# Kernel optimization log

Measured on AMD Instinct MI355X. Metric: run time of the kernel, lower is better.

The kernel has to match this reference:

```python
import jax, jax.numpy as jnp
import numpy as np

N_QUBITS = 12
K_STEPS = 6
VOCAB = 32000
D_EMB = 512
N_CLASSES = 8
B = 256
SEQ = 128
DIM = 2 ** N_QUBITS


def apply_1q(psi, U, q):
    # psi: [B, 2^n]; U: [2,2] (shared) or [B,2,2] (per-sample). Apply on wire q
    # (PennyLane convention: wire 0 = most significant axis).
    b = psi.shape[0]
    left, right = 2 ** q, 2 ** (N_QUBITS - q - 1)
    st = psi.reshape(b, left, 2, right)
    if U.ndim == 3:
        st = jnp.einsum('bij,bajr->bair', U, st)
    else:
        st = jnp.einsum('ij,bajr->bair', U, st)
    return st.reshape(b, DIM)


def apply_cnot(psi, c, t):
    b = psi.shape[0]
    st = psi.reshape((b,) + (2,) * N_QUBITS)
    c_ax, t_ax = 1 + c, 1 + t
    c0 = jnp.take(st, 0, axis=c_ax)
    c1 = jnp.take(st, 1, axis=c_ax)
    t_ax2 = t_ax - 1 if t_ax > c_ax else t_ax  # axis shift after take
    c1 = jnp.flip(c1, axis=t_ax2)
    return jnp.stack([c0, c1], axis=c_ax).reshape(b, DIM)


def ry_mat(angle):
    # angle: [B] -> [B,2,2] complex64
    c = jnp.cos(angle / 2)
    s = jnp.sin(angle / 2)
    row0 = jnp.stack([c, -s], axis=-1)
    row1 = jnp.stack([s, c], axis=-1)
    return jnp.stack([row0, row1], axis=-2).astype(jnp.complex64)


def rot_mat(phi, theta, omega):
    # PennyLane Rot(phi, theta, omega) = RZ(omega) RY(theta) RZ(phi)
    c = jnp.cos(theta / 2)
    s = jnp.sin(theta / 2)
    ep = jnp.exp(-0.5j * (phi + omega).astype(jnp.complex64))
    em = jnp.exp(0.5j * (phi - omega).astype(jnp.complex64))
    m = jnp.stack([jnp.stack([ep * c, -em * s]), jnp.stack([jnp.conj(em) * s, jnp.conj(ep) * c])])
    return m.astype(jnp.complex64)


def block(psi, x, theta_k):
    # data reupload RY(x_i), trainable Rot, ring of CNOTs (noiseless)
    for i in range(N_QUBITS):
        psi = apply_1q(psi, ry_mat(x[:, i]), i)
    for i in range(N_QUBITS):
        psi = apply_1q(psi, rot_mat(theta_k[i, 0], theta_k[i, 1], theta_k[i, 2]), i)
    for i in range(N_QUBITS - 1):
        psi = apply_cnot(psi, i, i + 1)
    psi = apply_cnot(psi, N_QUBITS - 1, 0)
    return psi


def z_expvals(psi):
    # <Z_i> for all wires from |psi|^2
    b = psi.shape[0]
    p = (psi.real ** 2 + psi.imag ** 2).reshape((b,) + (2,) * N_QUBITS)
    zs = []
    for i in range(N_QUBITS):
        axes = tuple(ax for ax in range(1, N_QUBITS + 1) if ax != 1 + i)
        m = p.sum(axis=axes)  # [B,2]
        zs.append(m[:, 0] - m[:, 1])
    return jnp.stack(zs, axis=-1)  # [B, n_qubits]


def _forward(input_ids, attention_mask, emb_table, proj_w, proj_b, theta, head_w, head_b):
    # encoder: embed -> masked mean pool -> tanh(linear) * pi
    e = emb_table[input_ids]                              # [B,S,D]
    mask = attention_mask[:, :, None].astype(jnp.float32)
    pooled = (e * mask).sum(axis=1) / jnp.clip(mask.sum(axis=1), 1.0)
    x = jnp.tanh(pooled @ proj_w.T + proj_b) * jnp.float32(np.pi)  # [B, n_qubits]

    b = x.shape[0]
    psi = jnp.zeros((b, DIM), jnp.complex64).at[:, 0].set(1.0)
    readouts = []
    for k in range(K_STEPS):
        psi = block(psi, x, theta[k])
        readouts.append(z_expvals(psi))
    step_readouts = jnp.stack(readouts, axis=0)           # [K,B,n_qubits]
    step_logits = step_readouts @ head_w.T + head_b       # [K,B,n_classes]
    return step_logits, step_readouts, step_logits[-1]


def setup_inputs() -> dict:
    key = jax.random.key(0)
    ks = jax.random.split(key, 6)
    input_ids = jax.random.randint(ks[0], (B, SEQ), 0, VOCAB)
    attention_mask = jnp.ones((B, SEQ), dtype=jnp.int32)
    emb_table = jax.random.normal(ks[1], (VOCAB, D_EMB), jnp.float32)
    emb_table = emb_table.at[0].set(0.0)  # padding_idx=0 row is zeros
    proj_w = jax.random.normal(ks[2], (N_QUBITS, D_EMB), jnp.float32) / np.sqrt(D_EMB)
    proj_b = jnp.zeros((N_QUBITS,), jnp.float32)
    theta = 0.01 * jax.random.normal(ks[3], (K_STEPS, N_QUBITS, 3), jnp.float32)
    head_w = jax.random.normal(ks[4], (N_CLASSES, N_QUBITS), jnp.float32) / np.sqrt(N_QUBITS)
    head_b = jnp.zeros((N_CLASSES,), jnp.float32)
    return {'input_ids': input_ids, 'attention_mask': attention_mask,
            'emb_table': emb_table, 'proj_w': proj_w, 'proj_b': proj_b,
            'theta': theta, 'head_w': head_w, 'head_b': head_b}


def reference(input_ids, attention_mask, emb_table, proj_w, proj_b, theta, head_w, head_b):
    return _forward(input_ids, attention_mask, emb_table, proj_w, proj_b, theta, head_w, head_b)
```

## Files before the change

### kernel.cpp

```cpp
#include <hip/hip_runtime.h>
#include <math.h>

#define NQ 12
#define DIM 4096
#define KS 6
#define BB 256
#define SEQ 128
#define DEMB 512


#define RG(P, W) { \
    float4 c0 = *(const float4*)&s_u[k][W][0]; \
    float4 c1 = *(const float4*)&s_u[k][W][4]; \
    float u00r=c0.x,u00i=c0.y,u01r=c0.z,u01i=c0.w; \
    float u10r=c1.x,u10i=c1.y,u11r=c1.z,u11i=c1.w; \
    _Pragma("unroll") \
    for (int r0 = 0; r0 < 8; ++r0) if (!(r0 & (1 << (P)))) { \
        int r1 = r0 | (1 << (P)); \
        float2 A = a[r0], Bv = a[r1]; \
        a[r0].x = u00r*A.x - u00i*A.y + u01r*Bv.x - u01i*Bv.y; \
        a[r0].y = u00r*A.y + u00i*A.x + u01r*Bv.y + u01i*Bv.x; \
        a[r1].x = u10r*A.x - u10i*A.y + u11r*Bv.x - u11i*Bv.y; \
        a[r1].y = u10r*A.y + u10i*A.x + u11r*Bv.y + u11i*Bv.x; \
    } }

#define SWAPB(lo, hi, M) { \
    float tx_ = (lane & M) ? lo.x : hi.x; \
    float ty_ = (lane & M) ? lo.y : hi.y; \
    tx_ = __shfl_xor(tx_, M, 64); \
    ty_ = __shfl_xor(ty_, M, 64); \
    if (lane & M) { lo.x = tx_; lo.y = ty_; } \
    else          { hi.x = tx_; hi.y = ty_; } \
}

#define BF_PLAIN(v, m) { float p_ = __shfl_xor(v, m, 64); v = v + p_; }
#define BF_SIGN(v, m)  { float p_ = __shfl_xor(v, m, 64); float d_ = v - p_; \
                         v = (lane & m) ? -d_ : d_; }

__device__ __forceinline__ int swz14(int x) { return x ^ ((x >> 4) & 14); }

__global__ __launch_bounds__(512) void fused_kernel(
    const int* __restrict__ ids, const int* __restrict__ mask,
    const float* __restrict__ emb, const float* __restrict__ pw,
    const float* __restrict__ pb, const float* __restrict__ theta,
    const float* __restrict__ hw, const float* __restrict__ hb,
    float* __restrict__ readouts, float* __restrict__ logits,
    float* __restrict__ last)
{
    __shared__ __align__(16) float2 buf0[DIM];
    __shared__ __align__(16) float2 buf1[DIM];
    __shared__ __align__(16) float  s_u[KS][NQ][8];
    __shared__ float  s_red[8][NQ];
    __shared__ float  s_msum[4];
    __shared__ float  s_wred[2][NQ];
    __shared__ float  s_x[NQ];
    __shared__ float  s_hw[8 * NQ];
    __shared__ float  s_hb[8];

    int b = blockIdx.x;
    int tid = threadIdx.x;
    int lane = tid & 63, wave = tid >> 6;

    int*   s_ids = (int*)buf1;
    float* s_m   = (float*)buf1 + SEQ;
    float4* s_part = (float4*)buf0;

    if (tid < SEQ) {
        s_ids[tid] = ids[b * SEQ + tid];
        s_m[tid]   = (float)mask[b * SEQ + tid];
    }
    if (tid >= 256 && tid < 256 + 8 * NQ) s_hw[tid - 256] = hw[tid - 256];
    if (tid >= 384 && tid < 392)          s_hb[tid - 384] = hb[tid - 384];
    __syncthreads();

    {
        int g = tid >> 7, e = tid & 127;
        float4 acc = make_float4(0.f, 0.f, 0.f, 0.f);
        float msum = 0.f;
        #pragma unroll 4
        for (int s = g; s < SEQ; s += 4) {
            float m = s_m[s];
            float4 v = ((const float4*)emb)[(size_t)s_ids[s] * 128 + e];
            acc.x = fmaf(m, v.x, acc.x);
            acc.y = fmaf(m, v.y, acc.y);
            acc.z = fmaf(m, v.z, acc.z);
            acc.w = fmaf(m, v.w, acc.w);
            msum += m;
        }
        __syncthreads();
        s_part[g * 128 + e] = acc;
        if (e == 0) s_msum[g] = msum;
    }
    __syncthreads();

    if (tid < 128) {
        float tm = fmaxf(s_msum[0] + s_msum[1] + s_msum[2] + s_msum[3], 1.f);
        float inv = 1.f / tm;
        float4 p0 = s_part[0 * 128 + tid], p1 = s_part[1 * 128 + tid];
        float4 p2 = s_part[2 * 128 + tid], p3 = s_part[3 * 128 + tid];
        float4 p;
        p.x = (p0.x + p1.x + p2.x + p3.x) * inv;
        p.y = (p0.y + p1.y + p2.y + p3.y) * inv;
        p.z = (p0.z + p1.z + p2.z + p3.z) * inv;
        p.w = (p0.w + p1.w + p2.w + p3.w) * inv;
        float z[NQ];
        #pragma unroll
        for (int i = 0; i < NQ; ++i) {
            float4 w4 = ((const float4*)pw)[i * 128 + tid];
            z[i] = p.x * w4.x + p.y * w4.y + p.z * w4.z + p.w * w4.w;
        }
        #pragma unroll
        for (int i = 0; i < NQ; ++i) {
            #pragma unroll
            for (int off = 32; off > 0; off >>= 1)
                z[i] += __shfl_xor(z[i], off, 64);
        }
        if ((tid & 63) == 0) {
            int w = tid >> 6;
            #pragma unroll
            for (int i = 0; i < NQ; ++i) s_wred[w][i] = z[i];
        }
    }
    __syncthreads();
    if (tid < NQ) {
        float d = pb[tid] + s_wred[0][tid] + s_wred[1][tid];
        s_x[tid] = tanhf(d) * 3.14159274101257324f;
    }
    __syncthreads();

    if (tid < KS * NQ * 4) {
        int k = tid / 48;
        int rem = tid - k * 48;
        int w = rem >> 2, q = rem & 3;
        float ang = s_x[w];
        float cy = cosf(0.5f * ang), sy = sinf(0.5f * ang);
        const float* th = theta + (k * NQ + w) * 3;
        float phi = th[0], te = th[1], om = th[2];
        float ct = cosf(0.5f * te), st = sinf(0.5f * te);
        float a1 = -0.5f * (phi + om);
        float a2 =  0.5f * (phi - om);
        float ar =  cosf(a1) * ct, ai =  sinf(a1) * ct;
        float br = -cosf(a2) * st, bi = -sinf(a2) * st;
        float x1 = (q & 1) ? ai : ar;
        float x2 = (q & 1) ? bi : br;
        float E  = (q & 2) ? (x2 * cy - x1 * sy) : (x1 * cy + x2 * sy);
        s_u[k][w][q] = E;
        s_u[k][w][(q & 2) ? q + 2 : q + 6] = (q == 1 || q == 2) ? -E : E;
    }

    int T8 = tid << 3;
    int baseA  = swz14(T8);
    int baseA4 = baseA >> 1;
    int addrC[8], addrD[8], idxP[8];
    #pragma unroll
    for (int r = 0; r < 8; ++r) {
        addrC[r] = swz14(lane + 64 * r + 512 * wave);
        int jD   = lane + 64 * wave + 512 * r;
        addrD[r] = swz14(jD);
        int b0 = (jD >> 11) & 1;
        int pref = b0, outv = 0;
        for (int w = 1; w < NQ; ++w) {
            pref ^= (jD >> (11 - w)) & 1;
            outv |= pref << (11 - w);
        }
        outv |= (b0 ^ pref) << 11;
        idxP[r] = swz14(outv);
    }
    int w0b = wave & 1, w1b = (wave >> 1) & 1, w2b = (wave >> 2) & 1;
    int wall = w0b ^ w1b ^ w2b;

    float2 a[8];
    #pragma unroll
    for (int r = 0; r < 8; ++r) a[r] = make_float2(0.f, 0.f);
    if (tid == 0) a[0].x = 1.f;
    __syncthreads();

    for (int k = 0; k < KS; ++k) {
        RG(0, 11) RG(1, 10) RG(2, 9)

        SWAPB(a[0], a[1], 1) SWAPB(a[2], a[3], 1)
        SWAPB(a[4], a[5], 1) SWAPB(a[6], a[7], 1)
        SWAPB(a[0], a[2], 2) SWAPB(a[1], a[3], 2)
        SWAPB(a[4], a[6], 2) SWAPB(a[5], a[7], 2)
        SWAPB(a[0], a[4], 4) SWAPB(a[1], a[5], 4)
        SWAPB(a[2], a[6], 4) SWAPB(a[3], a[7], 4)

        RG(0, 8) RG(1, 7) RG(2, 6)

        SWAPB(a[0], a[1], 8)  SWAPB(a[2], a[3], 8)
        SWAPB(a[4], a[5], 8)  SWAPB(a[6], a[7], 8)
        SWAPB(a[0], a[2], 16) SWAPB(a[1], a[3], 16)
        SWAPB(a[4], a[6], 16) SWAPB(a[5], a[7], 16)
        SWAPB(a[0], a[4], 32) SWAPB(a[1], a[5], 32)
        SWAPB(a[2], a[6], 32) SWAPB(a[3], a[7], 32)

        RG(0, 5) RG(1, 4) RG(2, 3)

        #pragma unroll
        for (int r = 0; r < 8; ++r) buf0[addrC[r]] = a[r];
        __syncthreads();
        #pragma unroll
        for (int r = 0; r < 8; ++r) a[r] = buf0[addrD[r]];

        RG(0, 2) RG(1, 1) RG(2, 0)

        #pragma unroll
        for (int r = 0; r < 8; ++r) buf1[idxP[r]] = a[r];

        {
            float p[8];
            #pragma unroll
            for (int r = 0; r < 8; ++r)
                p[r] = a[r].x * a[r].x + a[r].y * a[r].y;
            float Q1 = (p[0]+p[1]+p[6]+p[7]) - (p[2]+p[3]+p[4]+p[5]);
            float Q2 = (p[0]+p[3]+p[5]+p[6]) - (p[1]+p[2]+p[4]+p[7]);
            float Q0 = (p[0]+p[3]+p[4]+p[7]) - (p[1]+p[2]+p[5]+p[6]);
            float q1 = Q1, q2p = Q2, q0 = Q0;
            BF_PLAIN(q1,32) BF_PLAIN(q1,16) BF_PLAIN(q1,8)
            BF_PLAIN(q1,4)  BF_PLAIN(q1,2)  BF_PLAIN(q1,1)
            BF_PLAIN(q2p,32) BF_PLAIN(q2p,16) BF_PLAIN(q2p,8)
            BF_PLAIN(q2p,4)  BF_PLAIN(q2p,2)  BF_PLAIN(q2p,1)
            BF_SIGN(q0,32) BF_SIGN(q0,16) BF_SIGN(q0,8)
            BF_SIGN(q0,4)  BF_SIGN(q0,2)  BF_SIGN(q0,1)
            float c = Q2;
            BF_SIGN(c,32);
            float w6v = c; BF_PLAIN(w6v,16) BF_PLAIN(w6v,8) BF_PLAIN(w6v,4)
                           BF_PLAIN(w6v,2)  BF_PLAIN(w6v,1)
            BF_SIGN(c,16);
            float w7v = c; BF_PLAIN(w7v,8) BF_PLAIN(w7v,4)
                           BF_PLAIN(w7v,2) BF_PLAIN(w7v,1)
            BF_SIGN(c,8);
            float w8v = c; BF_PLAIN(w8v,4) BF_PLAIN(w8v,2) BF_PLAIN(w8v,1)
            BF_SIGN(c,4);
            float w9v = c; BF_PLAIN(w9v,2) BF_PLAIN(w9v,1)
            BF_SIGN(c,2);
            float w10v = c; BF_PLAIN(w10v,1)
            BF_SIGN(c,1);
            if (lane == 0) {
                float* sr = s_red[wave];
                sr[0]  = wall ? -q0  : q0;
                sr[1]  = q1;
                sr[2]  = q2p;
                sr[3]  = w2b ? -q2p : q2p;
                sr[4]  = (w1b ^ w2b) ? -q2p : q2p;
                sr[5]  = wall ? -q2p : q2p;
                sr[6]  = wall ? -w6v : w6v;
                sr[7]  = wall ? -w7v : w7v;
                sr[8]  = wall ? -w8v : w8v;
                sr[9]  = wall ? -w9v : w9v;
                sr[10] = wall ? -w10v : w10v;
                sr[11] = wall ? -c   : c;
            }
        }

        __syncthreads();
        #pragma unroll
        for (int i = 0; i < 4; ++i) {
            float4 v = ((float4*)buf1)[baseA4 ^ i];
            a[2*i]   = make_float2(v.x, v.y);
            a[2*i+1] = make_float2(v.z, v.w);
        }

        if (tid < NQ) {
            float s = 0.f;
            #pragma unroll
            for (int w2 = 0; w2 < 8; ++w2) s += s_red[w2][tid];
            readouts[(k * BB + b) * NQ + tid] = s;
        }
        if (tid < 8) {
            float acc2 = s_hb[tid];
            #pragma unroll
            for (int i = 0; i < NQ; ++i) {
                float si = 0.f;
                #pragma unroll
                for (int w2 = 0; w2 < 8; ++w2) si += s_red[w2][i];
                acc2 = fmaf(si, s_hw[tid * NQ + i], acc2);
            }
            logits[(k * BB + b) * 8 + tid] = acc2;
            if (k == KS - 1) last[b * 8 + tid] = acc2;
        }
    }
}

extern "C" void kernel_launch(void* const* d_in, const int* in_sizes, int n_in,
                              void* d_out, int out_size, void* d_ws, size_t ws_size,
                              hipStream_t stream) {
    const int*   ids   = (const int*)d_in[0];
    const int*   mask  = (const int*)d_in[1];
    const float* emb   = (const float*)d_in[2];
    const float* pw    = (const float*)d_in[3];
    const float* pb    = (const float*)d_in[4];
    const float* theta = (const float*)d_in[5];
    const float* hw    = (const float*)d_in[6];
    const float* hb    = (const float*)d_in[7];
    float* out = (float*)d_out;

    float* readouts = out + KS * BB * 8;
    float* last     = out + KS * BB * 8 + KS * BB * NQ;

    fused_kernel<<<BB, 512, 0, stream>>>(ids, mask, emb, pw, pb, theta,
                                         hw, hb, readouts, out, last);
}
```

Measured before the change: 141.7 us.

## Replace shuffle-based qubit swaps with wave-local LDS transposes and packed-FMA gates

Swaps the butterfly-style cross-lane shuffles (24 SWAPB shuffles per stage pair) for wave-private LDS round trips through buf0, using new swizzled address maps and a wave-level lgkmcnt wait in place of a block barrier. It also rewrites the 2x2 complex gate apply with float2 vector types, so the compiler can emit packed FP32 FMAs, and keeps only four unique unitary entries in shared memory. The aim is to cut shuffle instruction count and ALU work per gate. In exchange each stage adds LDS traffic and relies on wave-only visibility, so nothing can sync across waves.

```diff
diff --git a/kernel.cpp b/kernel.cpp
--- a/kernel.cpp
+++ b/kernel.cpp
@@ -9,33 +9,29 @@
 #define DEMB 512
 
 
+typedef float f2 __attribute__((ext_vector_type(2)));
+
 #define RG(P, W) { \
-    float4 c0 = *(const float4*)&s_u[k][W][0]; \
-    float4 c1 = *(const float4*)&s_u[k][W][4]; \
-    float u00r=c0.x,u00i=c0.y,u01r=c0.z,u01i=c0.w; \
-    float u10r=c1.x,u10i=c1.y,u11r=c1.z,u11i=c1.w; \
+    f2 E01 = *(const f2*)&s_u[k][W][0]; \
+    f2 E23 = *(const f2*)&s_u[k][W][2]; \
+    f2 PR0 = (f2){ E01.x,  E01.x}; \
+    f2 PI0 = (f2){-E01.y,  E01.y}; \
+    f2 PR1 = (f2){ E23.x,  E23.x}; \
+    f2 PI1 = (f2){-E23.y,  E23.y}; \
     _Pragma("unroll") \
     for (int r0 = 0; r0 < 8; ++r0) if (!(r0 & (1 << (P)))) { \
         int r1 = r0 | (1 << (P)); \
-        float2 A = a[r0], Bv = a[r1]; \
-        a[r0].x = u00r*A.x - u00i*A.y + u01r*Bv.x - u01i*Bv.y; \
-        a[r0].y = u00r*A.y + u00i*A.x + u01r*Bv.y + u01i*Bv.x; \
-        a[r1].x = u10r*A.x - u10i*A.y + u11r*Bv.x - u11i*Bv.y; \
-        a[r1].y = u10r*A.y + u10i*A.x + u11r*Bv.y + u11i*Bv.x; \
+        f2 A = a[r0], Bv = a[r1]; \
+        f2 As = (f2){A.y, A.x}, Bs = (f2){Bv.y, Bv.x}; \
+        a[r0] = PR0*A  + PI0*As + PR1*Bv + PI1*Bs; \
+        a[r1] = PR0*Bv - PI0*Bs - PR1*A  + PI1*As; \
     } }
-
-#define SWAPB(lo, hi, M) { \
-    float tx_ = (lane & M) ? lo.x : hi.x; \
-    float ty_ = (lane & M) ? lo.y : hi.y; \
-    tx_ = __shfl_xor(tx_, M, 64); \
-    ty_ = __shfl_xor(ty_, M, 64); \
-    if (lane & M) { lo.x = tx_; lo.y = ty_; } \
-    else          { hi.x = tx_; hi.y = ty_; } \
-}
 
 #define BF_PLAIN(v, m) { float p_ = __shfl_xor(v, m, 64); v = v + p_; }
 #define BF_SIGN(v, m)  { float p_ = __shfl_xor(v, m, 64); float d_ = v - p_; \
                          v = (lane & m) ? -d_ : d_; }
+
+#define WAVE_FENCE() asm volatile("s_waitcnt lgkmcnt(0)" ::: "memory")
 
 __device__ __forceinline__ int swz14(int x) { return x ^ ((x >> 4) & 14); }
 
@@ -47,9 +43,9 @@
     float* __restrict__ readouts, float* __restrict__ logits,
     float* __restrict__ last)
 {
-    __shared__ __align__(16) float2 buf0[DIM];
-    __shared__ __align__(16) float2 buf1[DIM];
-    __shared__ __align__(16) float  s_u[KS][NQ][8];
+    __shared__ __align__(16) f2    buf0[DIM];
+    __shared__ __align__(16) f2    buf1[DIM];
+    __shared__ __align__(16) float s_u[KS][NQ][4];
     __shared__ float  s_red[8][NQ];
     __shared__ float  s_msum[4];
     __shared__ float  s_wred[2][NQ];
@@ -145,15 +141,15 @@
         float x2 = (q & 1) ? bi : br;
         float E  = (q & 2) ? (x2 * cy - x1 * sy) : (x1 * cy + x2 * sy);
         s_u[k][w][q] = E;
-        s_u[k][w][(q & 2) ? q + 2 : q + 6] = (q == 1 || q == 2) ? -E : E;
     }
 
     int T8 = tid << 3;
     int baseA  = swz14(T8);
     int baseA4 = baseA >> 1;
-    int addrC[8], addrD[8], idxP[8];
+    int addrB[8], addrC[8], addrD[8], idxP[8];
     #pragma unroll
     for (int r = 0; r < 8; ++r) {
+        addrB[r] = swz14((lane & 7) + 8 * r + 64 * (lane >> 3) + 512 * wave);
         addrC[r] = swz14(lane + 64 * r + 512 * wave);
         int jD   = lane + 64 * wave + 512 * r;
         addrD[r] = swz14(jD);
@@ -169,30 +165,30 @@
     int w0b = wave & 1, w1b = (wave >> 1) & 1, w2b = (wave >> 2) & 1;
     int wall = w0b ^ w1b ^ w2b;
 
-    float2 a[8];
+    f2 a[8];
     #pragma unroll
-    for (int r = 0; r < 8; ++r) a[r] = make_float2(0.f, 0.f);
+    for (int r = 0; r < 8; ++r) a[r] = (f2){0.f, 0.f};
     if (tid == 0) a[0].x = 1.f;
     __syncthreads();
 
     for (int k = 0; k < KS; ++k) {
         RG(0, 11) RG(1, 10) RG(2, 9)
 
-        SWAPB(a[0], a[1], 1) SWAPB(a[2], a[3], 1)
-        SWAPB(a[4], a[5], 1) SWAPB(a[6], a[7], 1)
-        SWAPB(a[0], a[2], 2) SWAPB(a[1], a[3], 2)
-        SWAPB(a[4], a[6], 2) SWAPB(a[5], a[7], 2)
-        SWAPB(a[0], a[4], 4) SWAPB(a[1], a[5], 4)
-        SWAPB(a[2], a[6], 4) SWAPB(a[3], a[7], 4)
+        #pragma unroll
+        for (int i = 0; i < 4; ++i)
+            ((float4*)buf0)[baseA4 ^ i] =
+                make_float4(a[2*i].x, a[2*i].y, a[2*i+1].x, a[2*i+1].y);
+        WAVE_FENCE();
+        #pragma unroll
+        for (int r = 0; r < 8; ++r) a[r] = buf0[addrB[r]];
 
         RG(0, 8) RG(1, 7) RG(2, 6)
 
-        SWAPB(a[0], a[1], 8)  SWAPB(a[2], a[3], 8)
-        SWAPB(a[4], a[5], 8)  SWAPB(a[6], a[7], 8)
-        SWAPB(a[0], a[2], 16) SWAPB(a[1], a[3], 16)
-        SWAPB(a[4], a[6], 16) SWAPB(a[5], a[7], 16)
-        SWAPB(a[0], a[4], 32) SWAPB(a[1], a[5], 32)
-        SWAPB(a[2], a[6], 32) SWAPB(a[3], a[7], 32)
+        #pragma unroll
+        for (int r = 0; r < 8; ++r) buf0[addrB[r]] = a[r];
+        WAVE_FENCE();
+        #pragma unroll
+        for (int r = 0; r < 8; ++r) a[r] = buf0[addrC[r]];
 
         RG(0, 5) RG(1, 4) RG(2, 3)
 
@@ -257,8 +253,8 @@
         #pragma unroll
         for (int i = 0; i < 4; ++i) {
             float4 v = ((float4*)buf1)[baseA4 ^ i];
-            a[2*i]   = make_float2(v.x, v.y);
-            a[2*i+1] = make_float2(v.z, v.w);
+            a[2*i]   = (f2){v.x, v.y};
+            a[2*i+1] = (f2){v.z, v.w};
         }
 
         if (tid < NQ) {
```

After: 130.5 us. 7.9% less time.
